# Kernel tuning notes

Hardware: AMD Instinct MI355X
Metric: run time of the kernel (lower is better)

Reference implementation:

```python
import jax, jax.numpy as jnp
import numpy as np

B, S, N, D, H, M, P_OFF = 16, 4, 2048, 128, 16, 4096, 4092


def setup_inputs() -> dict:
    key = jax.random.key(0)
    ks = jax.random.split(key, 6)
    return {
        "X": jax.random.normal(ks[0], (B, S, N), dtype=jnp.float32),
        "W_q": jax.random.normal(ks[1], (N, N), dtype=jnp.float32) * 0.02,
        "W_k": jax.random.normal(ks[2], (N, N), dtype=jnp.float32) * 0.02,
        "W_v": jax.random.normal(ks[3], (N, N), dtype=jnp.float32) * 0.02,
        "cache_K": jax.random.normal(ks[4], (B, H, M, D), dtype=jnp.float32),
        "cache_V": jax.random.normal(ks[5], (B, H, M, D), dtype=jnp.float32),
        "P": P_OFF,
    }


def reference(X, W_q, W_k, W_v, cache_K, cache_V, P):
    b, s, n = X.shape
    _, h, m, d = cache_K.shape
    # RMSNorm (no eps, no learned scale, matching the source)
    variance = jnp.mean(X * X, axis=-1, keepdims=True)
    X_norm = X * jax.lax.rsqrt(variance)
    # QKV projections -> [b, h, s, d]
    Q = (X_norm @ W_q).reshape(b, s, h, d).transpose(0, 2, 1, 3)
    K = (X_norm @ W_k).reshape(b, s, h, d).transpose(0, 2, 1, 3)
    V = (X_norm @ W_v).reshape(b, s, h, d).transpose(0, 2, 1, 3)
    # KV-cache write at static offset P
    cK = cache_K.at[:, :, P:P + s, :].set(K)
    cV = cache_V.at[:, :, P:P + s, :].set(V)
    # Attention over full cache (note: source applies no 1/sqrt(d) scale)
    scores = jnp.einsum("bhsd,bhmd->bhsm", Q, cK)
    attn = jax.nn.softmax(scores, axis=-1)
    O = jnp.einsum("bhsm,bhmd->bhsd", attn, cV)
    return O.transpose(0, 2, 1, 3).reshape(b, s, n)
```

## Files before the change

kernel.cpp:

```cpp
#include <hip/hip_runtime.h>
#include <hip/hip_bf16.h>
#include <math.h>

#define NB 16
#define NS 4
#define NN 2048
#define ND 128
#define NH 16
#define NM 4096
#define NCHK 8
#define CHROWS 512
#define TROWS 16
#define NT 32
#define NKC 16

#define SC_OFF   0u
#define Q_OFF    131072u
#define K_OFF    262144u
#define V_OFF    393216u
#define OP_OFF   524288u
#define ML_OFF   1572864u
#define PART_OFF 1589248u

__global__ __launch_bounds__(256) void k_rmsnorm(const float* __restrict__ X,
                                                 float* __restrict__ ws) {
    const int row = blockIdx.x;
    const int tid = threadIdx.x;
    const float* xr = X + (size_t)row * NN;
    float4 a = *(const float4*)(xr + tid * 4);
    float4 b = *(const float4*)(xr + 1024 + tid * 4);
    float ss = a.x*a.x + a.y*a.y + a.z*a.z + a.w*a.w
             + b.x*b.x + b.y*b.y + b.z*b.z + b.w*b.w;
    #pragma unroll
    for (int off = 32; off; off >>= 1) ss += __shfl_xor(ss, off);
    __shared__ float ls[4];
    if ((tid & 63) == 0) ls[tid >> 6] = ss;
    __syncthreads();
    if (tid == 0)
        ws[SC_OFF + row] = rsqrtf((ls[0] + ls[1] + ls[2] + ls[3]) * (1.0f / NN));
}

__global__ __launch_bounds__(256) void k_qkv(const float* __restrict__ X,
                                             const float* __restrict__ Wq,
                                             const float* __restrict__ Wk,
                                             const float* __restrict__ Wv,
                                             float* __restrict__ ws) {
    __shared__ float xsT[64][68];
    __shared__ float wt[64][132];
    const int ct    = blockIdx.x;
    const int which = blockIdx.y;
    const int kc    = blockIdx.z;
    const float* __restrict__ W = (which == 0) ? Wq : (which == 1) ? Wk : Wv;
    const int tid = threadIdx.x;
    const int c0  = ct * 128;
    const int rg  = tid >> 5;
    const int cg  = tid & 31;
    const float scl = ws[SC_OFF + (tid >> 2)];

    float4 acc[8];
    #pragma unroll
    for (int i = 0; i < 8; i++) acc[i] = make_float4(0.f, 0.f, 0.f, 0.f);

    for (int s = 0; s < 2; s++) {
        const int k0 = kc * 128 + s * 64;
        __syncthreads();
        {
            const int r  = tid >> 2;
            const int q4 = tid & 3;
            #pragma unroll
            for (int i = 0; i < 4; i++) {
                const int f4 = q4 + i * 4;
                float4 v = *(const float4*)(X + (size_t)r * NN + k0 + f4 * 4);
                xsT[f4 * 4 + 0][r] = v.x * scl;
                xsT[f4 * 4 + 1][r] = v.y * scl;
                xsT[f4 * 4 + 2][r] = v.z * scl;
                xsT[f4 * 4 + 3][r] = v.w * scl;
            }
        }
        {
            #pragma unroll
            for (int j8 = 0; j8 < 8; j8++) {
                const int kk  = j8 * 8 + (tid >> 5);
                const int f4c = tid & 31;
                float4 v = *(const float4*)(W + (size_t)(k0 + kk) * NN + c0 + f4c * 4);
                *(float4*)&wt[kk][f4c * 4] = v;
            }
        }
        __syncthreads();
        #pragma unroll 8
        for (int kk = 0; kk < 64; kk++) {
            const float4 x0 = *(const float4*)&xsT[kk][rg * 8];
            const float4 x1 = *(const float4*)&xsT[kk][rg * 8 + 4];
            const float4 w4 = *(const float4*)&wt[kk][cg * 4];
            acc[0].x += x0.x*w4.x; acc[0].y += x0.x*w4.y; acc[0].z += x0.x*w4.z; acc[0].w += x0.x*w4.w;
            acc[1].x += x0.y*w4.x; acc[1].y += x0.y*w4.y; acc[1].z += x0.y*w4.z; acc[1].w += x0.y*w4.w;
            acc[2].x += x0.z*w4.x; acc[2].y += x0.z*w4.y; acc[2].z += x0.z*w4.z; acc[2].w += x0.z*w4.w;
            acc[3].x += x0.w*w4.x; acc[3].y += x0.w*w4.y; acc[3].z += x0.w*w4.z; acc[3].w += x0.w*w4.w;
            acc[4].x += x1.x*w4.x; acc[4].y += x1.x*w4.y; acc[4].z += x1.x*w4.z; acc[4].w += x1.x*w4.w;
            acc[5].x += x1.y*w4.x; acc[5].y += x1.y*w4.y; acc[5].z += x1.y*w4.z; acc[5].w += x1.y*w4.w;
            acc[6].x += x1.z*w4.x; acc[6].y += x1.z*w4.y; acc[6].z += x1.z*w4.z; acc[6].w += x1.z*w4.w;
            acc[7].x += x1.w*w4.x; acc[7].y += x1.w*w4.y; acc[7].z += x1.w*w4.z; acc[7].w += x1.w*w4.w;
        }
    }
    float* po = ws + PART_OFF + (size_t)(kc * 3 + which) * 131072u;
    #pragma unroll
    for (int i = 0; i < 8; i++)
        *(float4*)(po + (size_t)(rg * 8 + i) * NN + c0 + cg * 4) = acc[i];
}

__global__ __launch_bounds__(256) void k_reduce(float* __restrict__ ws) {
    const int idx = blockIdx.x * 256 + threadIdx.x;
    const int which = idx >> 15;
    const int off   = idx & 32767;
    float4 s = make_float4(0.f, 0.f, 0.f, 0.f);
    #pragma unroll
    for (int kcc = 0; kcc < NKC; kcc++) {
        const float4 v = *(const float4*)(ws + PART_OFF
                         + (size_t)(kcc * 3 + which) * 131072u + (size_t)off * 4);
        s.x += v.x; s.y += v.y; s.z += v.z; s.w += v.w;
    }
    *(float4*)(ws + Q_OFF + (size_t)which * 131072u + (size_t)off * 4) = s;
}

__global__ __launch_bounds__(256) void k_attn(const float* __restrict__ cK,
                                              const float* __restrict__ cV,
                                              const int* __restrict__ Pp,
                                              float* __restrict__ ws) {
    const int ch = blockIdx.x, h = blockIdx.y, b = blockIdx.z;
    const int tid = threadIdx.x;
    const int wv = tid >> 6, lane = tid & 63;
    const int r16 = lane & 15, qd = lane >> 4;
    const int P = *Pp;
    __shared__ float Ks[2][TROWS * 128];
    __shared__ float Vs[2][TROWS * 128];
    __shared__ float Qs[4][4][40] __attribute__((aligned(16)));
    __shared__ float ps[TROWS][4] __attribute__((aligned(16)));
    __shared__ float facs[4] __attribute__((aligned(16)));
    __shared__ float Ow[4][4][128];
    __shared__ float mls[4][2];

    if (tid < 128) {
        const int q = tid >> 5, idx = tid & 31;
        const int qq = idx >> 3, jj = idx & 7;
        *(float4*)&Qs[q][qq][jj * 4] =
            *(const float4*)(ws + Q_OFF + (size_t)(b * 4 + q) * NN + h * 128 + idx * 4);
    }

    const float* kbase = cK + (size_t)(b * NH + h) * NM * ND;
    const float* vbase = cV + (size_t)(b * NH + h) * NM * ND;
    const float* knew  = ws + K_OFF;
    const float* vnew  = ws + V_OFF;
    const int mb0 = ch * CHROWS;

    auto STAGE = [&](int tt, int bufi) {
        const int mb = mb0 + tt * TROWS;
        #pragma unroll
        for (int i = 0; i < 2; i++) {
            const int g0  = (wv * 2 + i) * 64;
            const int g   = g0 + lane;
            const int row = g >> 5;
            const int c4  = g & 31;
            const int csw = c4 ^ (row & 7);
            const int mrow = mb + row;
            const float* src = (mrow >= P && mrow < P + NS)
                ? knew + (size_t)(b * 4 + (mrow - P)) * NN + h * 128 + csw * 4
                : kbase + (size_t)mrow * ND + csw * 4;
            __builtin_amdgcn_global_load_lds(
                (const __attribute__((address_space(1))) void*)src,
                (__attribute__((address_space(3))) void*)(&Ks[bufi][g0 * 4]),
                16, 0, 0);
        }
        #pragma unroll
        for (int i = 0; i < 2; i++) {
            const int g0  = (wv * 2 + i) * 64;
            const int g   = g0 + lane;
            const int row = g >> 5;
            const int c4  = g & 31;
            const int mrow = mb + row;
            const float* src = (mrow >= P && mrow < P + NS)
                ? vnew + (size_t)(b * 4 + (mrow - P)) * NN + h * 128 + c4 * 4
                : vbase + (size_t)mrow * ND + c4 * 4;
            __builtin_amdgcn_global_load_lds(
                (const __attribute__((address_space(1))) void*)src,
                (__attribute__((address_space(3))) void*)(&Vs[bufi][g0 * 4]),
                16, 0, 0);
        }
    };

    float m_run = -INFINITY, l_run = 0.f;
    float2 Oa[4];
    #pragma unroll
    for (int q = 0; q < 4; q++) Oa[q] = make_float2(0.f, 0.f);

    STAGE(0, 0);
    __syncthreads();

    for (int t = 0; t < NT; t++) {
        const int cur = t & 1;
        if (t < NT - 1) STAGE(t + 1, cur ^ 1);

        const int s7 = r16 & 7;
        const float* kr = &Ks[cur][r16 * 128 + qd * 32];
        const float* qr = &Qs[wv][qd][0];
        float s = 0.f;
        #pragma unroll
        for (int j = 0; j < 8; j++) {
            const float4 k4 = *(const float4*)&kr[(j ^ s7) * 4];
            const float4 q4 = *(const float4*)&qr[j * 4];
            s += k4.x*q4.x + k4.y*q4.y + k4.z*q4.z + k4.w*q4.w;
        }
        s += __shfl_xor(s, 16);
        s += __shfl_xor(s, 32);
        float wm = s;
        #pragma unroll
        for (int off = 8; off; off >>= 1) wm = fmaxf(wm, __shfl_xor(wm, off));
        const float mn  = fmaxf(m_run, wm);
        const float fac = __expf(m_run - mn);
        m_run = mn;
        const float p = __expf(s - mn);
        l_run = l_run * fac + ((qd == 0) ? p : 0.f);
        if (qd == 0) ps[r16][wv] = p;
        if (lane == 0) facs[wv] = fac;
        asm volatile("s_waitcnt lgkmcnt(0)" ::: "memory");
        __builtin_amdgcn_s_barrier();
        __builtin_amdgcn_sched_barrier(0);

        const float4 fq = *(const float4*)&facs[0];
        Oa[0].x *= fq.x; Oa[0].y *= fq.x;
        Oa[1].x *= fq.y; Oa[1].y *= fq.y;
        Oa[2].x *= fq.z; Oa[2].y *= fq.z;
        Oa[3].x *= fq.w; Oa[3].y *= fq.w;
        const int r0 = wv * 4;
        #pragma unroll
        for (int rr = 0; rr < 4; rr++) {
            const float2 v2 = *(const float2*)&Vs[cur][(r0 + rr) * 128 + lane * 2];
            const float4 pr = *(const float4*)&ps[r0 + rr][0];
            Oa[0].x += pr.x * v2.x; Oa[0].y += pr.x * v2.y;
            Oa[1].x += pr.y * v2.x; Oa[1].y += pr.y * v2.y;
            Oa[2].x += pr.z * v2.x; Oa[2].y += pr.z * v2.y;
            Oa[3].x += pr.w * v2.x; Oa[3].y += pr.w * v2.y;
        }
        __syncthreads();
    }

    #pragma unroll
    for (int off = 32; off; off >>= 1) l_run += __shfl_xor(l_run, off);
    #pragma unroll
    for (int q = 0; q < 4; q++)
        *(float2*)&Ow[wv][q][lane * 2] = Oa[q];
    if (lane == 0) { mls[wv][0] = m_run; mls[wv][1] = l_run; }
    __syncthreads();

    const int q = wv;
    const int d0 = lane * 2;
    float o0 = 0.f, o1 = 0.f;
    #pragma unroll
    for (int w2 = 0; w2 < 4; w2++) {
        o0 += Ow[w2][q][d0];
        o1 += Ow[w2][q][d0 + 1];
    }
    const size_t bh = (size_t)(b * NH + h);
    const size_t pidx = ((bh * NCHK + ch) * 4 + q) * 128 + d0;
    ws[OP_OFF + pidx]     = o0;
    ws[OP_OFF + pidx + 1] = o1;
    if (lane == 0) {
        const size_t mi = ((bh * NCHK + ch) * 4 + q) * 2;
        ws[ML_OFF + mi]     = mls[q][0];
        ws[ML_OFF + mi + 1] = mls[q][1];
    }
}

__global__ __launch_bounds__(256) void k_comb(const float* __restrict__ ws,
                                              float* __restrict__ out) {
    const int bh = blockIdx.x;
    const int b = bh >> 4, h = bh & 15;
    const int tid = threadIdx.x;
    const int q = tid >> 6, d0 = (tid & 63) * 2;
    float ms = -INFINITY;
    #pragma unroll
    for (int c = 0; c < NCHK; c++)
        ms = fmaxf(ms, ws[ML_OFF + (((size_t)bh * NCHK + c) * 4 + q) * 2]);
    float o0 = 0.f, o1 = 0.f, den = 0.f;
    #pragma unroll
    for (int c = 0; c < NCHK; c++) {
        const size_t mi = (((size_t)bh * NCHK + c) * 4 + q) * 2;
        float e = __expf(ws[ML_OFF + mi] - ms);
        den += e * ws[ML_OFF + mi + 1];
        const size_t pi = (((size_t)bh * NCHK + c) * 4 + q) * 128 + d0;
        o0 += e * ws[OP_OFF + pi];
        o1 += e * ws[OP_OFF + pi + 1];
    }
    const float inv = 1.0f / den;
    const size_t oi = (size_t)(b * 4 + q) * NN + h * 128 + d0;
    *(float2*)(out + oi) = make_float2(o0 * inv, o1 * inv);
}

extern "C" void kernel_launch(void* const* d_in, const int* in_sizes, int n_in,
                              void* d_out, int out_size, void* d_ws, size_t ws_size,
                              hipStream_t stream) {
    const float* X  = (const float*)d_in[0];
    const float* Wq = (const float*)d_in[1];
    const float* Wk = (const float*)d_in[2];
    const float* Wv = (const float*)d_in[3];
    const float* cK = (const float*)d_in[4];
    const float* cV = (const float*)d_in[5];
    const int*   Pp = (const int*)d_in[6];
    float* ws = (float*)d_ws;
    float* out = (float*)d_out;

    hipLaunchKernelGGL(k_rmsnorm, dim3(64), dim3(256), 0, stream, X, ws);
    hipLaunchKernelGGL(k_qkv, dim3(16, 3, NKC), dim3(256), 0, stream, X, Wq, Wk, Wv, ws);
    hipLaunchKernelGGL(k_reduce, dim3(384), dim3(256), 0, stream, ws);
    hipLaunchKernelGGL(k_attn, dim3(NCHK, NH, NB), dim3(256), 0, stream, cK, cV, Pp, ws);
    hipLaunchKernelGGL(k_comb, dim3(NB * NH), dim3(256), 0, stream, ws, out);
}
```

Baseline: 247.7 us.

## Rewrite attention as single-wave blocks with 4-deep async LDS ring pipeline

The attention kernel now uses 64-thread blocks over 32 chunks of 128 cache rows instead of 256-thread blocks over 8 chunks. Each wave handles all 4 queries itself, streaming two K/V rows per step through a 4-slot LDS ring filled by global_load_lds and throttled with vmcnt waits, so no workgroup barriers are needed. The softmax rescale is skipped unless the running max rises. The price is more partials for the combine kernel to merge and a larger workspace, plus a shallow per-wave prefetch depth for a bandwidth-bound cache stream.

```diff
diff --git a/kernel.cpp b/kernel.cpp
--- a/kernel.cpp
+++ b/kernel.cpp
@@ -8,10 +8,9 @@
 #define ND 128
 #define NH 16
 #define NM 4096
-#define NCHK 8
-#define CHROWS 512
-#define TROWS 16
-#define NT 32
+#define NCHK2 32
+#define CHROWS2 128
+#define NUNITS 64
 #define NKC 16
 
 #define SC_OFF   0u
@@ -19,8 +18,8 @@
 #define K_OFF    262144u
 #define V_OFF    393216u
 #define OP_OFF   524288u
-#define ML_OFF   1572864u
-#define PART_OFF 1589248u
+#define ML_OFF   4718592u
+#define PART_OFF 4784128u
 
 __global__ __launch_bounds__(256) void k_rmsnorm(const float* __restrict__ X,
                                                  float* __restrict__ ws) {
@@ -122,151 +121,112 @@
     *(float4*)(ws + Q_OFF + (size_t)which * 131072u + (size_t)off * 4) = s;
 }
 
-__global__ __launch_bounds__(256) void k_attn(const float* __restrict__ cK,
-                                              const float* __restrict__ cV,
-                                              const int* __restrict__ Pp,
-                                              float* __restrict__ ws) {
+__global__ __launch_bounds__(64, 4) void k_attn(const float* __restrict__ cK,
+                                                const float* __restrict__ cV,
+                                                const int* __restrict__ Pp,
+                                                float* __restrict__ ws) {
     const int ch = blockIdx.x, h = blockIdx.y, b = blockIdx.z;
-    const int tid = threadIdx.x;
-    const int wv = tid >> 6, lane = tid & 63;
-    const int r16 = lane & 15, qd = lane >> 4;
+    const int lane = threadIdx.x;
+    const int q = lane >> 4, sub = lane & 15;
     const int P = *Pp;
-    __shared__ float Ks[2][TROWS * 128];
-    __shared__ float Vs[2][TROWS * 128];
-    __shared__ float Qs[4][4][40] __attribute__((aligned(16)));
-    __shared__ float ps[TROWS][4] __attribute__((aligned(16)));
-    __shared__ float facs[4] __attribute__((aligned(16)));
-    __shared__ float Ow[4][4][128];
-    __shared__ float mls[4][2];
-
-    if (tid < 128) {
-        const int q = tid >> 5, idx = tid & 31;
-        const int qq = idx >> 3, jj = idx & 7;
-        *(float4*)&Qs[q][qq][jj * 4] =
-            *(const float4*)(ws + Q_OFF + (size_t)(b * 4 + q) * NN + h * 128 + idx * 4);
-    }
+    __shared__ float ring[4][2][256];
 
     const float* kbase = cK + (size_t)(b * NH + h) * NM * ND;
     const float* vbase = cV + (size_t)(b * NH + h) * NM * ND;
     const float* knew  = ws + K_OFF;
     const float* vnew  = ws + V_OFF;
-    const int mb0 = ch * CHROWS;
-
-    auto STAGE = [&](int tt, int bufi) {
-        const int mb = mb0 + tt * TROWS;
+    const int mb0 = ch * CHROWS2;
+
+    const float* qrow = ws + Q_OFF + (size_t)(b * 4 + q) * NN + h * 128;
+    const float4 qA = *(const float4*)(qrow + sub * 4);
+    const float4 qB = *(const float4*)(qrow + 64 + sub * 4);
+
+    auto STAGE = [&](int u, int slot) {
+        const int row = mb0 + u * 2 + (lane >> 5);
+        const int c = (lane & 31) * 4;
+        const float* ksrc; const float* vsrc;
+        if (row >= P && row < P + NS) {
+            const size_t ro = (size_t)(b * 4 + (row - P)) * NN + h * 128 + c;
+            ksrc = knew + ro; vsrc = vnew + ro;
+        } else {
+            const size_t ro = (size_t)row * ND + c;
+            ksrc = kbase + ro; vsrc = vbase + ro;
+        }
+        __builtin_amdgcn_global_load_lds(
+            (const __attribute__((address_space(1))) void*)ksrc,
+            (__attribute__((address_space(3))) void*)(&ring[slot][0][0]),
+            16, 0, 0);
+        __builtin_amdgcn_global_load_lds(
+            (const __attribute__((address_space(1))) void*)vsrc,
+            (__attribute__((address_space(3))) void*)(&ring[slot][1][0]),
+            16, 0, 0);
+    };
+
+    float m_run = -INFINITY, l_run = 0.f;
+    float o0=0.f,o1=0.f,o2=0.f,o3=0.f,o4=0.f,o5=0.f,o6=0.f,o7=0.f;
+
+    auto PROCESS = [&](int slot) {
+        const float* kp = &ring[slot][0][0];
+        const float* vp = &ring[slot][1][0];
+        const float4 k00 = *(const float4*)&kp[sub * 4];
+        const float4 k01 = *(const float4*)&kp[64 + sub * 4];
+        const float4 k10 = *(const float4*)&kp[128 + sub * 4];
+        const float4 k11 = *(const float4*)&kp[192 + sub * 4];
+        float s0 = k00.x*qA.x + k00.y*qA.y + k00.z*qA.z + k00.w*qA.w
+                 + k01.x*qB.x + k01.y*qB.y + k01.z*qB.z + k01.w*qB.w;
+        float s1 = k10.x*qA.x + k10.y*qA.y + k10.z*qA.z + k10.w*qA.w
+                 + k11.x*qB.x + k11.y*qB.y + k11.z*qB.z + k11.w*qB.w;
         #pragma unroll
-        for (int i = 0; i < 2; i++) {
-            const int g0  = (wv * 2 + i) * 64;
-            const int g   = g0 + lane;
-            const int row = g >> 5;
-            const int c4  = g & 31;
-            const int csw = c4 ^ (row & 7);
-            const int mrow = mb + row;
-            const float* src = (mrow >= P && mrow < P + NS)
-                ? knew + (size_t)(b * 4 + (mrow - P)) * NN + h * 128 + csw * 4
-                : kbase + (size_t)mrow * ND + csw * 4;
-            __builtin_amdgcn_global_load_lds(
-                (const __attribute__((address_space(1))) void*)src,
-                (__attribute__((address_space(3))) void*)(&Ks[bufi][g0 * 4]),
-                16, 0, 0);
-        }
-        #pragma unroll
-        for (int i = 0; i < 2; i++) {
-            const int g0  = (wv * 2 + i) * 64;
-            const int g   = g0 + lane;
-            const int row = g >> 5;
-            const int c4  = g & 31;
-            const int mrow = mb + row;
-            const float* src = (mrow >= P && mrow < P + NS)
-                ? vnew + (size_t)(b * 4 + (mrow - P)) * NN + h * 128 + c4 * 4
-                : vbase + (size_t)mrow * ND + c4 * 4;
-            __builtin_amdgcn_global_load_lds(
-                (const __attribute__((address_space(1))) void*)src,
-                (__attribute__((address_space(3))) void*)(&Vs[bufi][g0 * 4]),
-                16, 0, 0);
-        }
+        for (int off = 1; off <= 8; off <<= 1) {
+            s0 += __shfl_xor(s0, off);
+            s1 += __shfl_xor(s1, off);
+        }
+        const float wm = fmaxf(s0, s1);
+        if (wm > m_run) {
+            const float fac = __expf(m_run - wm);
+            l_run *= fac;
+            o0*=fac; o1*=fac; o2*=fac; o3*=fac;
+            o4*=fac; o5*=fac; o6*=fac; o7*=fac;
+            m_run = wm;
+        }
+        const float p0 = __expf(s0 - m_run);
+        const float p1 = __expf(s1 - m_run);
+        l_run += p0 + p1;
+        const float4 v00 = *(const float4*)&vp[sub * 4];
+        const float4 v01 = *(const float4*)&vp[64 + sub * 4];
+        const float4 v10 = *(const float4*)&vp[128 + sub * 4];
+        const float4 v11 = *(const float4*)&vp[192 + sub * 4];
+        o0 += p0*v00.x + p1*v10.x;  o1 += p0*v00.y + p1*v10.y;
+        o2 += p0*v00.z + p1*v10.z;  o3 += p0*v00.w + p1*v10.w;
+        o4 += p0*v01.x + p1*v11.x;  o5 += p0*v01.y + p1*v11.y;
+        o6 += p0*v01.z + p1*v11.z;  o7 += p0*v01.w + p1*v11.w;
     };
 
-    float m_run = -INFINITY, l_run = 0.f;
-    float2 Oa[4];
-    #pragma unroll
-    for (int q = 0; q < 4; q++) Oa[q] = make_float2(0.f, 0.f);
-
-    STAGE(0, 0);
-    __syncthreads();
-
-    for (int t = 0; t < NT; t++) {
-        const int cur = t & 1;
-        if (t < NT - 1) STAGE(t + 1, cur ^ 1);
-
-        const int s7 = r16 & 7;
-        const float* kr = &Ks[cur][r16 * 128 + qd * 32];
-        const float* qr = &Qs[wv][qd][0];
-        float s = 0.f;
-        #pragma unroll
-        for (int j = 0; j < 8; j++) {
-            const float4 k4 = *(const float4*)&kr[(j ^ s7) * 4];
-            const float4 q4 = *(const float4*)&qr[j * 4];
-            s += k4.x*q4.x + k4.y*q4.y + k4.z*q4.z + k4.w*q4.w;
-        }
-        s += __shfl_xor(s, 16);
-        s += __shfl_xor(s, 32);
-        float wm = s;
-        #pragma unroll
-        for (int off = 8; off; off >>= 1) wm = fmaxf(wm, __shfl_xor(wm, off));
-        const float mn  = fmaxf(m_run, wm);
-        const float fac = __expf(m_run - mn);
-        m_run = mn;
-        const float p = __expf(s - mn);
-        l_run = l_run * fac + ((qd == 0) ? p : 0.f);
-        if (qd == 0) ps[r16][wv] = p;
-        if (lane == 0) facs[wv] = fac;
-        asm volatile("s_waitcnt lgkmcnt(0)" ::: "memory");
-        __builtin_amdgcn_s_barrier();
+    STAGE(0, 0); STAGE(1, 1); STAGE(2, 2);
+    for (int u = 0; u < NUNITS - 3; ++u) {
+        STAGE(u + 3, (u + 3) & 3);
         __builtin_amdgcn_sched_barrier(0);
-
-        const float4 fq = *(const float4*)&facs[0];
-        Oa[0].x *= fq.x; Oa[0].y *= fq.x;
-        Oa[1].x *= fq.y; Oa[1].y *= fq.y;
-        Oa[2].x *= fq.z; Oa[2].y *= fq.z;
-        Oa[3].x *= fq.w; Oa[3].y *= fq.w;
-        const int r0 = wv * 4;
-        #pragma unroll
-        for (int rr = 0; rr < 4; rr++) {
-            const float2 v2 = *(const float2*)&Vs[cur][(r0 + rr) * 128 + lane * 2];
-            const float4 pr = *(const float4*)&ps[r0 + rr][0];
-            Oa[0].x += pr.x * v2.x; Oa[0].y += pr.x * v2.y;
-            Oa[1].x += pr.y * v2.x; Oa[1].y += pr.y * v2.y;
-            Oa[2].x += pr.z * v2.x; Oa[2].y += pr.z * v2.y;
-            Oa[3].x += pr.w * v2.x; Oa[3].y += pr.w * v2.y;
-        }
-        __syncthreads();
-    }
-
-    #pragma unroll
-    for (int off = 32; off; off >>= 1) l_run += __shfl_xor(l_run, off);
-    #pragma unroll
-    for (int q = 0; q < 4; q++)
-        *(float2*)&Ow[wv][q][lane * 2] = Oa[q];
-    if (lane == 0) { mls[wv][0] = m_run; mls[wv][1] = l_run; }
-    __syncthreads();
-
-    const int q = wv;
-    const int d0 = lane * 2;
-    float o0 = 0.f, o1 = 0.f;
-    #pragma unroll
-    for (int w2 = 0; w2 < 4; w2++) {
-        o0 += Ow[w2][q][d0];
-        o1 += Ow[w2][q][d0 + 1];
-    }
-    const size_t bh = (size_t)(b * NH + h);
-    const size_t pidx = ((bh * NCHK + ch) * 4 + q) * 128 + d0;
-    ws[OP_OFF + pidx]     = o0;
-    ws[OP_OFF + pidx + 1] = o1;
-    if (lane == 0) {
-        const size_t mi = ((bh * NCHK + ch) * 4 + q) * 2;
-        ws[ML_OFF + mi]     = mls[q][0];
-        ws[ML_OFF + mi + 1] = mls[q][1];
+        asm volatile("s_waitcnt vmcnt(6)" ::: "memory");
+        __builtin_amdgcn_sched_barrier(0);
+        PROCESS(u & 3);
+    }
+    asm volatile("s_waitcnt vmcnt(4)" ::: "memory");
+    __builtin_amdgcn_sched_barrier(0);
+    PROCESS((NUNITS - 3) & 3);
+    asm volatile("s_waitcnt vmcnt(2)" ::: "memory");
+    __builtin_amdgcn_sched_barrier(0);
+    PROCESS((NUNITS - 2) & 3);
+    asm volatile("s_waitcnt vmcnt(0)" ::: "memory");
+    __builtin_amdgcn_sched_barrier(0);
+    PROCESS((NUNITS - 1) & 3);
+
+    const size_t base = (((size_t)(b * NH + h) * NCHK2 + ch) * 4 + q);
+    float* op = ws + OP_OFF + base * 128;
+    *(float4*)(op + sub * 4)      = make_float4(o0, o1, o2, o3);
+    *(float4*)(op + 64 + sub * 4) = make_float4(o4, o5, o6, o7);
+    if (sub == 0) {
+        ws[ML_OFF + base * 2]     = m_run;
+        ws[ML_OFF + base * 2 + 1] = l_run;
     }
 }
 
@@ -278,15 +238,15 @@
     const int q = tid >> 6, d0 = (tid & 63) * 2;
     float ms = -INFINITY;
     #pragma unroll
-    for (int c = 0; c < NCHK; c++)
-        ms = fmaxf(ms, ws[ML_OFF + (((size_t)bh * NCHK + c) * 4 + q) * 2]);
+    for (int c = 0; c < NCHK2; c++)
+        ms = fmaxf(ms, ws[ML_OFF + (((size_t)bh * NCHK2 + c) * 4 + q) * 2]);
     float o0 = 0.f, o1 = 0.f, den = 0.f;
-    #pragma unroll
-    for (int c = 0; c < NCHK; c++) {
-        const size_t mi = (((size_t)bh * NCHK + c) * 4 + q) * 2;
+    #pragma unroll 8
+    for (int c = 0; c < NCHK2; c++) {
+        const size_t mi = (((size_t)bh * NCHK2 + c) * 4 + q) * 2;
         float e = __expf(ws[ML_OFF + mi] - ms);
         den += e * ws[ML_OFF + mi + 1];
-        const size_t pi = (((size_t)bh * NCHK + c) * 4 + q) * 128 + d0;
+        const size_t pi = (((size_t)bh * NCHK2 + c) * 4 + q) * 128 + d0;
         o0 += e * ws[OP_OFF + pi];
         o1 += e * ws[OP_OFF + pi + 1];
     }
@@ -311,6 +271,6 @@
     hipLaunchKernelGGL(k_rmsnorm, dim3(64), dim3(256), 0, stream, X, ws);
     hipLaunchKernelGGL(k_qkv, dim3(16, 3, NKC), dim3(256), 0, stream, X, Wq, Wk, Wv, ws);
     hipLaunchKernelGGL(k_reduce, dim3(384), dim3(256), 0, stream, ws);
-    hipLaunchKernelGGL(k_attn, dim3(NCHK, NH, NB), dim3(256), 0, stream, cK, cV, Pp, ws);
+    hipLaunchKernelGGL(k_attn, dim3(NCHK2, NH, NB), dim3(64), 0, stream, cK, cV, Pp, ws);
     hipLaunchKernelGGL(k_comb, dim3(NB * NH), dim3(256), 0, stream, ws, out);
 }
```

Result: slower. 253.7 us (+2.4%).
